# Kernel optimization log

Hardware: AMD Instinct MI355X
Metric: run time of the kernel (lower is better)

The kernel has to match this reference:

```python
import jax, jax.numpy as jnp
import numpy as np

B, S, NCH, OUT = 16384, 256, 8, 2
EPS = 1e-5

def setup_inputs() -> dict:
    key = jax.random.key(0)
    ks = jax.random.split(key, 8)
    scale = 1.0 / np.sqrt(S)
    x = jax.random.normal(ks[0], (B, S, 2 * NCH), dtype=jnp.float32)
    h_0 = jnp.zeros((1,), dtype=jnp.float32)
    # per-channel complex linear weights, stacked: [n_channels, out=S, in=S]
    Wr = jax.random.normal(ks[1], (NCH, S, S), dtype=jnp.float32) * scale
    Wi = jax.random.normal(ks[2], (NCH, S, S), dtype=jnp.float32) * scale
    # final complex linear: [out=OUT//2, in=NCH*S]
    Wfr = jax.random.normal(ks[3], (OUT // 2, NCH * S), dtype=jnp.float32) / np.sqrt(NCH * S)
    Wfi = jax.random.normal(ks[4], (OUT // 2, NCH * S), dtype=jnp.float32) / np.sqrt(NCH * S)
    g_in = jnp.ones((2 * NCH,), dtype=jnp.float32)
    b_in = jnp.zeros((2 * NCH,), dtype=jnp.float32)
    g_out = jnp.ones((OUT,), dtype=jnp.float32)
    b_out = jnp.zeros((OUT,), dtype=jnp.float32)
    return {"x": x, "h_0": h_0, "Wr": Wr, "Wi": Wi, "Wfr": Wfr, "Wfi": Wfi,
            "g_in": g_in, "b_in": b_in, "g_out": g_out, "b_out": b_out}

def reference(x, h_0, Wr, Wi, Wfr, Wfi, g_in, b_in, g_out, b_out):
    # bn_in (training mode): x permuted to [B, 2n, S] in torch -> stats per feature over (B, S)
    mu = jnp.mean(x, axis=(0, 1))
    var = jnp.var(x, axis=(0, 1))  # biased, as torch uses for normalization
    xn = (x - mu) * jax.lax.rsqrt(var + EPS) * g_in + b_in  # [B, S, 2n]
    xi = xn[:, :, 0::2]  # [B, S, n] real parts
    xq = xn[:, :, 1::2]  # [B, S, n] imag parts
    # batched complex linear over channels: y[b,o,c] = sum_s x[b,s,c] W[c,o,s]
    cr = jnp.einsum('bsc,cos->boc', xi, Wr) - jnp.einsum('bsc,cos->boc', xq, Wi)
    ci = jnp.einsum('bsc,cos->boc', xq, Wr) + jnp.einsum('bsc,cos->boc', xi, Wi)
    amp2 = xi * xi + xq * xq  # [B, S, n]
    # channel blocks concatenated along last dim: channel-major ordering
    x_ii = jnp.transpose(amp2 * cr, (0, 2, 1)).reshape(B, NCH * S)
    x_qq = jnp.transpose(amp2 * ci, (0, 2, 1)).reshape(B, NCH * S)
    Cr = x_ii @ Wfr.T - x_qq @ Wfi.T  # [B, OUT//2]
    Ci = x_qq @ Wfr.T + x_ii @ Wfi.T
    y = jnp.concatenate([Cr, Ci], axis=-1)  # [B, OUT]
    mu2 = jnp.mean(y, axis=0)
    var2 = jnp.var(y, axis=0)
    return (y - mu2) * jax.lax.rsqrt(var2 + EPS) * g_out + b_out
```

## Files before the change

kernel.cpp:

```cpp
#include <hip/hip_runtime.h>
#include <stdint.h>

#define B_N   16384
#define S_N   256
#define NCH   8
#define P_N   (B_N * S_N)
#define EPS_F 1e-5f

typedef float  f32x4  __attribute__((ext_vector_type(4)));
typedef __bf16 bf16x8 __attribute__((ext_vector_type(8)));
typedef unsigned int u32x4 __attribute__((ext_vector_type(4)));
typedef unsigned int u32x2 __attribute__((ext_vector_type(2)));

static __device__ __forceinline__ unsigned short f2bf(float f) {
  union { float f; unsigned u; } v; v.f = f;
  unsigned u = v.u;
  u += 0x7fffu + ((u >> 16) & 1u);
  return (unsigned short)(u >> 16);
}
static __device__ __forceinline__ float bf2f(unsigned short h) {
  union { unsigned u; float f; } v; v.u = ((unsigned)h) << 16;
  return v.f;
}

typedef const __attribute__((address_space(1))) unsigned int* gas1_t;
typedef __attribute__((address_space(3))) unsigned int* las3_t;
static __device__ __forceinline__ void gl16(const void* g, void* l) {
  __builtin_amdgcn_global_load_lds((gas1_t)(uintptr_t)g,
                                   (las3_t)(unsigned int)(uintptr_t)l, 16, 0, 0);
}

__global__ __launch_bounds__(256) void pass1_kernel(
    const float* __restrict__ x, unsigned short* __restrict__ xplan,
    float* __restrict__ partials)
{
  __shared__ float ps[4][32];
  const int t = threadIdx.x;
  const int q = t & 3;
  const int pg = t >> 2;
  float s[4] = {0.f,0.f,0.f,0.f}, ss[4] = {0.f,0.f,0.f,0.f};
  const f32x4* xv = (const f32x4*)x;

  for (int it = 0; it < 4; ++it) {
    size_t p0 = ((size_t)blockIdx.x * 4 + it) * 512 + (size_t)pg * 8;
    f32x4 v[8];
    #pragma unroll
    for (int j = 0; j < 8; ++j) v[j] = xv[(p0 + j) * 4 + q];
    #pragma unroll
    for (int j = 0; j < 8; ++j)
      #pragma unroll
      for (int k = 0; k < 4; ++k) { s[k] += v[j][k]; ss[k] += v[j][k] * v[j][k]; }
    #pragma unroll
    for (int j2 = 0; j2 < 4; ++j2) {
      u32x4 w;
      #pragma unroll
      for (int k = 0; k < 4; ++k)
        w[k] = (unsigned)f2bf(v[2*k][j2]) | ((unsigned)f2bf(v[2*k+1][j2]) << 16);
      *(u32x4*)(xplan + (size_t)(q * 4 + j2) * P_N + p0) = w;
    }
  }

  #pragma unroll
  for (int off = 32; off >= 4; off >>= 1) {
    #pragma unroll
    for (int k = 0; k < 4; ++k) { s[k] += __shfl_down(s[k], off); ss[k] += __shfl_down(ss[k], off); }
  }
  const int lane = t & 63, wid = t >> 6;
  if (lane < 4) {
    #pragma unroll
    for (int k = 0; k < 4; ++k) {
      ps[wid][lane * 4 + k]      = s[k];
      ps[wid][16 + lane * 4 + k] = ss[k];
    }
  }
  __syncthreads();
  if (t < 32)
    partials[blockIdx.x * 32 + t] = ps[0][t] + ps[1][t] + ps[2][t] + ps[3][t];
}

__global__ __launch_bounds__(1024) void finalize_kernel(
    const float* __restrict__ partials, const float* __restrict__ g_in,
    const float* __restrict__ b_in, float* __restrict__ AC)
{
  __shared__ float acc[32][32];
  const int t = threadIdx.x;
  const int v = t & 31, chunk = t >> 5;
  float s = 0.f;
  for (int i = 0; i < 64; ++i)
    s += partials[(size_t)(chunk * 64 + i) * 32 + v];
  acc[chunk][v] = s;
  __syncthreads();
  if (t < 32) {
    float tot = 0.f;
    #pragma unroll
    for (int k = 0; k < 32; ++k) tot += acc[k][t];
    acc[0][t] = tot;
  }
  __syncthreads();
  if (t < 16) {
    float n = (float)P_N;
    float mu  = acc[0][t] / n;
    float var = acc[0][16 + t] / n - mu * mu;
    float A = g_in[t] * rsqrtf(var + EPS_F);
    AC[t] = A;
    AC[16 + t] = b_in[t] - mu * A;
  }
}

__global__ __launch_bounds__(256) void wprep_kernel(
    const float* __restrict__ Wr, const float* __restrict__ Wi,
    unsigned short* __restrict__ wr_bf, unsigned short* __restrict__ wi_bf,
    float* __restrict__ RWr, float* __restrict__ RWi)
{
  __shared__ float sr[4], si[4];
  const int row = blockIdx.x, t = threadIdx.x;
  const size_t idx = (size_t)row * 256 + t;
  float vr = Wr[idx], vi = Wi[idx];
  wr_bf[idx] = f2bf(vr);
  wi_bf[idx] = f2bf(vi);
  float rr = vr, ri = vi;
  #pragma unroll
  for (int off = 32; off >= 1; off >>= 1) { rr += __shfl_down(rr, off); ri += __shfl_down(ri, off); }
  if ((t & 63) == 0) { sr[t >> 6] = rr; si[t >> 6] = ri; }
  __syncthreads();
  if (t == 0) {
    RWr[row] = sr[0] + sr[1] + sr[2] + sr[3];
    RWi[row] = si[0] + si[1] + si[2] + si[3];
  }
}

__global__ __launch_bounds__(256) void kterm_kernel(
    const float* __restrict__ AC, const float* __restrict__ RWr, const float* __restrict__ RWi,
    float* __restrict__ Kr, float* __restrict__ Ki)
{
  int idx = blockIdx.x * 256 + threadIdx.x;
  int c = idx >> 8;
  float Ci_ = AC[16 + 2*c], Cq_ = AC[16 + 2*c + 1];
  Kr[idx] = Ci_ * RWr[idx] - Cq_ * RWi[idx];
  Ki[idx] = Cq_ * RWr[idx] + Ci_ * RWi[idx];
}

static __device__ __forceinline__ void issue_w(
    const unsigned short* __restrict__ wr_bf, const unsigned short* __restrict__ wi_bf,
    int c, int u, char* wbuf, int t)
{
  const int oh = u >> 3, c32 = u & 7;
  #pragma unroll
  for (int i = 0; i < 4; ++i) {
    const int L = i * 4096 + t * 16;
    const int row = i * 32 + (t >> 3);
    const int ds_ = (t & 7) ^ (row & 7);
    const unsigned short* wb = (ds_ & 4) ? wi_bf : wr_bf;
    const char* g = (const char*)(wb + (size_t)(c * 256 + oh * 128 + row) * 256
                                     + c32 * 32 + (ds_ & 3) * 8);
    gl16(g, wbuf + L);
  }
}

static __device__ __forceinline__ void issue_x(
    const unsigned short* __restrict__ xplan, int c, int b0, char* xlds, int t)
{
  #pragma unroll
  for (int i = 0; i < 8; ++i) {
    const int plane = i >> 2, si = i & 3;
    const int L = plane * 16384 + si * 4096 + t * 16;
    const int row = si * 8 + (t >> 5);
    const int gd = (t & 31) ^ (row & 7);
    const char* g = (const char*)xplan
        + (((size_t)(2 * c + plane) * P_N + (size_t)(b0 + row) * 256) << 1) + (gd << 4);
    gl16(g, xlds + L);
  }
}

__global__ __launch_bounds__(256, 2) void main_kernel(
    const unsigned short* __restrict__ xplan,
    const unsigned short* __restrict__ wr_bf,
    const unsigned short* __restrict__ wi_bf,
    const float* __restrict__ AC,
    const float* __restrict__ Kr, const float* __restrict__ Ki,
    const float* __restrict__ Wfr, const float* __restrict__ Wfi,
    float* __restrict__ y)
{
  __shared__ char Xlds[32768];
  __shared__ char Wlds[49152];
  float (*red)[32][2] = (float(*)[32][2])Wlds;

  const int t = threadIdx.x;
  const int wid = t >> 6, lane = t & 63;
  const int col = lane & 15, kg = lane >> 4;
  const int b0 = blockIdx.x * 32;

  float pCr[2][4], pCi[2][4];
  #pragma unroll
  for (int m = 0; m < 2; ++m)
    #pragma unroll
    for (int r = 0; r < 4; ++r) { pCr[m][r] = 0.f; pCi[m][r] = 0.f; }

  for (int c = 0; c < NCH; ++c) {
    __builtin_amdgcn_s_barrier();
    issue_x(xplan, c, b0, Xlds, t);
    issue_w(wr_bf, wi_bf, c, 0, Wlds, t);
    int wsel = 0;

    for (int oh = 0; oh < 2; ++oh) {
      f32x4 Srr[2][2], Sqi[2][2], Sqr[2][2], Sii[2][2];
      #pragma unroll
      for (int m = 0; m < 2; ++m)
        #pragma unroll
        for (int n = 0; n < 2; ++n) {
          Srr[m][n] = (f32x4){0.f,0.f,0.f,0.f};
          Sqi[m][n] = (f32x4){0.f,0.f,0.f,0.f};
          Sqr[m][n] = (f32x4){0.f,0.f,0.f,0.f};
          Sii[m][n] = (f32x4){0.f,0.f,0.f,0.f};
        }
      #pragma unroll
      for (int t7 = 0; t7 < 8; ++t7) {
        const int u = oh * 8 + t7;
        const int nsel = (wsel == 2) ? 0 : wsel + 1;
        if (u < 15) {
          issue_w(wr_bf, wi_bf, c, u + 1, Wlds + nsel * 16384, t);
          asm volatile("s_waitcnt vmcnt(4)" ::: "memory");
        } else {
          asm volatile("s_waitcnt vmcnt(0)" ::: "memory");
        }
        __builtin_amdgcn_s_barrier();
        __builtin_amdgcn_sched_barrier(0);

        const int axo = (((t7 * 4 + kg) ^ (col & 7)) << 4);
        bf16x8 ari0 = *(const bf16x8*)(Xlds + col * 512 + axo);
        bf16x8 ari1 = *(const bf16x8*)(Xlds + (16 + col) * 512 + axo);
        bf16x8 aqi0 = *(const bf16x8*)(Xlds + 16384 + col * 512 + axo);
        bf16x8 aqi1 = *(const bf16x8*)(Xlds + 16384 + (16 + col) * 512 + axo);
        const char* Wb = Wlds + wsel * 16384;
        #pragma unroll
        for (int nf = 0; nf < 2; ++nf) {
          const int r = wid * 32 + nf * 16 + col;
          bf16x8 br = *(const bf16x8*)(Wb + r * 128 + (((kg    ) ^ (r & 7)) << 4));
          bf16x8 bi = *(const bf16x8*)(Wb + r * 128 + (((kg + 4) ^ (r & 7)) << 4));
          Srr[0][nf] = __builtin_amdgcn_mfma_f32_16x16x32_bf16(ari0, br, Srr[0][nf], 0,0,0);
          Srr[1][nf] = __builtin_amdgcn_mfma_f32_16x16x32_bf16(ari1, br, Srr[1][nf], 0,0,0);
          Sqr[0][nf] = __builtin_amdgcn_mfma_f32_16x16x32_bf16(aqi0, br, Sqr[0][nf], 0,0,0);
          Sqr[1][nf] = __builtin_amdgcn_mfma_f32_16x16x32_bf16(aqi1, br, Sqr[1][nf], 0,0,0);
          Sii[0][nf] = __builtin_amdgcn_mfma_f32_16x16x32_bf16(ari0, bi, Sii[0][nf], 0,0,0);
          Sii[1][nf] = __builtin_amdgcn_mfma_f32_16x16x32_bf16(ari1, bi, Sii[1][nf], 0,0,0);
          Sqi[0][nf] = __builtin_amdgcn_mfma_f32_16x16x32_bf16(aqi0, bi, Sqi[0][nf], 0,0,0);
          Sqi[1][nf] = __builtin_amdgcn_mfma_f32_16x16x32_bf16(aqi1, bi, Sqi[1][nf], 0,0,0);
        }
        __builtin_amdgcn_sched_barrier(0);
        wsel = nsel;
      }

      const float Ai_ = AC[2*c],      Aq_ = AC[2*c + 1];
      const float Cin = AC[16 + 2*c], Cqn = AC[16 + 2*c + 1];
      #pragma unroll
      for (int nf = 0; nf < 2; ++nf) {
        const int o = oh * 128 + wid * 32 + nf * 16 + col;
        const int gidx = c * 256 + o;
        const float kr = Kr[gidx], ki = Ki[gidx];
        const float wfr = Wfr[gidx], wfi = Wfi[gidx];
        const int og = o >> 3, ob = (o & 7) * 2;
        #pragma unroll
        for (int mf = 0; mf < 2; ++mf) {
          const int bl = mf * 16 + kg * 4;
          #pragma unroll
          for (int r = 0; r < 4; ++r) {
            const int row = bl + r;
            const int sb = row * 512 + ((og ^ (row & 7)) << 4) + ob;
            float xiv = Ai_ * bf2f(*(const unsigned short*)(Xlds + sb)) + Cin;
            float xqv = Aq_ * bf2f(*(const unsigned short*)(Xlds + 16384 + sb)) + Cqn;
            float cr = Ai_ * Srr[mf][nf][r] - Aq_ * Sqi[mf][nf][r] + kr;
            float ci = Aq_ * Sqr[mf][nf][r] + Ai_ * Sii[mf][nf][r] + ki;
            float amp2 = xiv * xiv + xqv * xqv;
            pCr[mf][r] += amp2 * (cr * wfr - ci * wfi);
            pCi[mf][r] += amp2 * (ci * wfr + cr * wfi);
          }
        }
      }
    }
  }

  #pragma unroll
  for (int off = 1; off < 16; off <<= 1) {
    #pragma unroll
    for (int m = 0; m < 2; ++m)
      #pragma unroll
      for (int r = 0; r < 4; ++r) {
        pCr[m][r] += __shfl_xor(pCr[m][r], off);
        pCi[m][r] += __shfl_xor(pCi[m][r], off);
      }
  }
  __syncthreads();
  if (col == 0) {
    #pragma unroll
    for (int m = 0; m < 2; ++m)
      #pragma unroll
      for (int r = 0; r < 4; ++r) {
        red[wid][m*16 + kg*4 + r][0] = pCr[m][r];
        red[wid][m*16 + kg*4 + r][1] = pCi[m][r];
      }
  }
  __syncthreads();
  if (t < 64) {
    int bl = t >> 1, cc = t & 1;
    float v = red[0][bl][cc] + red[1][bl][cc] + red[2][bl][cc] + red[3][bl][cc];
    y[(size_t)(b0 + bl) * 2 + cc] = v;
  }
}

__global__ __launch_bounds__(1024) void ln_kernel(
    const float* __restrict__ y, const float* __restrict__ g_out, const float* __restrict__ b_out,
    float* __restrict__ out)
{
  __shared__ float wsum[16][4];
  __shared__ float st[4];
  const int t = threadIdx.x;
  float s0 = 0.f, q0 = 0.f, s1 = 0.f, q1 = 0.f;
  for (int r = t; r < B_N; r += 1024) {
    float v0 = y[2*r], v1 = y[2*r + 1];
    s0 += v0; q0 += v0 * v0;
    s1 += v1; q1 += v1 * v1;
  }
  #pragma unroll
  for (int off = 32; off >= 1; off >>= 1) {
    s0 += __shfl_down(s0, off); q0 += __shfl_down(q0, off);
    s1 += __shfl_down(s1, off); q1 += __shfl_down(q1, off);
  }
  if ((t & 63) == 0) { int w = t >> 6; wsum[w][0]=s0; wsum[w][1]=q0; wsum[w][2]=s1; wsum[w][3]=q1; }
  __syncthreads();
  if (t == 0) {
    float S0=0.f,Q0=0.f,S1=0.f,Q1=0.f;
    for (int w = 0; w < 16; ++w) { S0+=wsum[w][0]; Q0+=wsum[w][1]; S1+=wsum[w][2]; Q1+=wsum[w][3]; }
    float n = (float)B_N;
    float mu0 = S0 / n, var0 = Q0 / n - mu0 * mu0;
    float mu1 = S1 / n, var1 = Q1 / n - mu1 * mu1;
    st[0] = mu0; st[1] = rsqrtf(var0 + EPS_F);
    st[2] = mu1; st[3] = rsqrtf(var1 + EPS_F);
  }
  __syncthreads();
  float g0 = g_out[0], g1 = g_out[1], bo0 = b_out[0], bo1 = b_out[1];
  float mu0 = st[0], rs0 = st[1], mu1 = st[2], rs1 = st[3];
  for (int r = t; r < B_N; r += 1024) {
    out[2*r]     = (y[2*r]     - mu0) * rs0 * g0 + bo0;
    out[2*r + 1] = (y[2*r + 1] - mu1) * rs1 * g1 + bo1;
  }
}

extern "C" void kernel_launch(void* const* d_in, const int* in_sizes, int n_in,
                              void* d_out, int out_size, void* d_ws, size_t ws_size,
                              hipStream_t stream) {
  (void)in_sizes; (void)n_in; (void)out_size; (void)ws_size;
  const float* x    = (const float*)d_in[0];
  const float* Wr   = (const float*)d_in[2];
  const float* Wi   = (const float*)d_in[3];
  const float* Wfr  = (const float*)d_in[4];
  const float* Wfi  = (const float*)d_in[5];
  const float* g_in = (const float*)d_in[6];
  const float* b_in = (const float*)d_in[7];
  const float* g_out= (const float*)d_in[8];
  const float* b_out= (const float*)d_in[9];
  float* out = (float*)d_out;

  char* ws = (char*)d_ws;
  float* AC    = (float*)(ws + 128);
  float* RWr   = (float*)(ws + 256);
  float* RWi   = (float*)(ws + 256 + 8192);
  float* Kr    = (float*)(ws + 256 + 16384);
  float* Ki    = (float*)(ws + 256 + 24576);
  float* y     = (float*)(ws + 33024);
  float* partials = (float*)(ws + 164096);
  unsigned short* wr_bf = (unsigned short*)(ws + 164096);
  unsigned short* wi_bf = (unsigned short*)(ws + 164096 + 1048576);
  unsigned short* xplan = (unsigned short*)(ws + 2261248);

  pass1_kernel<<<2048, 256, 0, stream>>>(x, xplan, partials);
  finalize_kernel<<<1, 1024, 0, stream>>>(partials, g_in, b_in, AC);
  wprep_kernel<<<2048, 256, 0, stream>>>(Wr, Wi, wr_bf, wi_bf, RWr, RWi);
  kterm_kernel<<<8, 256, 0, stream>>>(AC, RWr, RWi, Kr, Ki);
  main_kernel<<<B_N / 32, 256, 0, stream>>>(xplan, wr_bf, wi_bf, AC, Kr, Ki, Wfr, Wfi, y);
  ln_kernel<<<1, 1024, 0, stream>>>(y, g_out, b_out, out);
}
```

Measured before the change: 201.8 us.

## Retile main kernel to 64-row blocks with unified X/W triple-buffered pipeline

The main kernel now processes 64 batch rows per 512-thread block, and each wave computes a 32x64 output tile. X and W chunks are streamed per 32-wide K phase through a 3-stage LDS ring, using a new interleaved real/imag weight layout written by wprep. Amplitude-squared values are precomputed once into LDS as bf16 rather than recomputed from the full X tile. This halves the weight reloads per batch row and overlaps the X loads with compute, at the cost of more LDS and registers per block, which may lower occupancy.

After: 218.8 us. +8.4%, slower.

```diff
diff --git a/kernel.cpp b/kernel.cpp
--- a/kernel.cpp
+++ b/kernel.cpp
@@ -9,6 +9,7 @@
 
 typedef float  f32x4  __attribute__((ext_vector_type(4)));
 typedef __bf16 bf16x8 __attribute__((ext_vector_type(8)));
+typedef __bf16 bf16x4 __attribute__((ext_vector_type(4)));
 typedef unsigned int u32x4 __attribute__((ext_vector_type(4)));
 typedef unsigned int u32x2 __attribute__((ext_vector_type(2)));
 
@@ -109,15 +110,18 @@
 
 __global__ __launch_bounds__(256) void wprep_kernel(
     const float* __restrict__ Wr, const float* __restrict__ Wi,
-    unsigned short* __restrict__ wr_bf, unsigned short* __restrict__ wi_bf,
+    unsigned short* __restrict__ wp,
     float* __restrict__ RWr, float* __restrict__ RWi)
 {
   __shared__ float sr[4], si[4];
   const int row = blockIdx.x, t = threadIdx.x;
+  const int c = row >> 8, o = row & 255;
   const size_t idx = (size_t)row * 256 + t;
   float vr = Wr[idx], vi = Wi[idx];
-  wr_bf[idx] = f2bf(vr);
-  wi_bf[idx] = f2bf(vi);
+  const int u = t >> 5, g = (t >> 3) & 3, j = t & 7;
+  const size_t base = ((size_t)((c * 8 + u) * 256 + o) << 6) + g * 8 + j;
+  wp[base]      = f2bf(vr);
+  wp[base + 32] = f2bf(vi);
   float rr = vr, ri = vi;
   #pragma unroll
   for (int off = 32; off >= 1; off >>= 1) { rr += __shfl_down(rr, off); ri += __shfl_down(ri, off); }
@@ -140,55 +144,53 @@
   Ki[idx] = Cq_ * RWr[idx] + Ci_ * RWi[idx];
 }
 
-static __device__ __forceinline__ void issue_w(
-    const unsigned short* __restrict__ wr_bf, const unsigned short* __restrict__ wi_bf,
-    int c, int u, char* wbuf, int t)
-{
-  const int oh = u >> 3, c32 = u & 7;
+static __device__ __forceinline__ void issue_phase(
+    const unsigned short* __restrict__ xplan, const unsigned short* __restrict__ wp,
+    int p, int b0, int t, char* xbuf, char* wbuf)
+{
+  const int c = p >> 3, u = p & 7;
+  {
+    const int row = t >> 3, slot = t & 7;
+    const int sd = slot ^ (row & 7);
+    const int pl = sd >> 2, g = sd & 3;
+    const char* gsrc = (const char*)xplan +
+        (((size_t)(2 * c + pl) * P_N + (size_t)(b0 + row) * 256 + u * 32 + g * 8) << 1);
+    gl16(gsrc, xbuf + t * 16);
+  }
   #pragma unroll
   for (int i = 0; i < 4; ++i) {
-    const int L = i * 4096 + t * 16;
-    const int row = i * 32 + (t >> 3);
-    const int ds_ = (t & 7) ^ (row & 7);
-    const unsigned short* wb = (ds_ & 4) ? wi_bf : wr_bf;
-    const char* g = (const char*)(wb + (size_t)(c * 256 + oh * 128 + row) * 256
-                                     + c32 * 32 + (ds_ & 3) * 8);
-    gl16(g, wbuf + L);
-  }
-}
-
-static __device__ __forceinline__ void issue_x(
-    const unsigned short* __restrict__ xplan, int c, int b0, char* xlds, int t)
-{
-  #pragma unroll
-  for (int i = 0; i < 8; ++i) {
-    const int plane = i >> 2, si = i & 3;
-    const int L = plane * 16384 + si * 4096 + t * 16;
-    const int row = si * 8 + (t >> 5);
-    const int gd = (t & 31) ^ (row & 7);
-    const char* g = (const char*)xplan
-        + (((size_t)(2 * c + plane) * P_N + (size_t)(b0 + row) * 256) << 1) + (gd << 4);
-    gl16(g, xlds + L);
-  }
-}
-
-__global__ __launch_bounds__(256, 2) void main_kernel(
+    const int o = i * 64 + (t >> 3), slot = t & 7;
+    const int gd = slot ^ (o & 7);
+    const char* gsrc = (const char*)wp +
+        (((size_t)((c * 8 + u) * 256 + o)) << 7) + (gd << 4);
+    gl16(gsrc, wbuf + i * 8192 + t * 16);
+  }
+}
+
+__global__ __launch_bounds__(512, 2) void main_kernel(
     const unsigned short* __restrict__ xplan,
-    const unsigned short* __restrict__ wr_bf,
-    const unsigned short* __restrict__ wi_bf,
+    const unsigned short* __restrict__ wp,
     const float* __restrict__ AC,
     const float* __restrict__ Kr, const float* __restrict__ Ki,
     const float* __restrict__ Wfr, const float* __restrict__ Wfi,
     float* __restrict__ y)
 {
-  __shared__ char Xlds[32768];
-  __shared__ char Wlds[49152];
-  float (*red)[32][2] = (float(*)[32][2])Wlds;
+  __shared__ char Xc[3][8192];
+  __shared__ char Wc[3][32768];
+  __shared__ unsigned short amp2s[64][256];
+  __shared__ float red[4][64][2];
+  __shared__ float acs[32];
 
   const int t = threadIdx.x;
   const int wid = t >> 6, lane = t & 63;
+  const int mw = wid >> 2, ow = wid & 3;
   const int col = lane & 15, kg = lane >> 4;
-  const int b0 = blockIdx.x * 32;
+  const int c7 = col & 7;
+  const int b0 = blockIdx.x * 64;
+  const int srow = t >> 3, aoq = t & 7;
+  const int ag = aoq >> 1, ah = aoq & 1;
+
+  if (t < 32) acs[t] = AC[t];
 
   float pCr[2][4], pCi[2][4];
   #pragma unroll
@@ -196,83 +198,98 @@
     #pragma unroll
     for (int r = 0; r < 4; ++r) { pCr[m][r] = 0.f; pCi[m][r] = 0.f; }
 
-  for (int c = 0; c < NCH; ++c) {
+  f32x4 acc[2][4][4];
+
+  issue_phase(xplan, wp, 0, b0, t, Xc[0], Wc[0]);
+  issue_phase(xplan, wp, 1, b0, t, Xc[1], Wc[1]);
+
+  float Ai_ = 0.f, Aq_ = 0.f, Cin = 0.f, Cqn = 0.f;
+
+  #pragma unroll 1
+  for (int p = 0; p < 64; ++p) {
+    const int c = p >> 3, u = p & 7;
+    if (p == 63) { asm volatile("s_waitcnt vmcnt(0)" ::: "memory"); }
+    else         { asm volatile("s_waitcnt vmcnt(5)" ::: "memory"); }
     __builtin_amdgcn_s_barrier();
-    issue_x(xplan, c, b0, Xlds, t);
-    issue_w(wr_bf, wi_bf, c, 0, Wlds, t);
-    int wsel = 0;
-
-    for (int oh = 0; oh < 2; ++oh) {
-      f32x4 Srr[2][2], Sqi[2][2], Sqr[2][2], Sii[2][2];
-      #pragma unroll
-      for (int m = 0; m < 2; ++m)
+    if (p + 2 < 64)
+      issue_phase(xplan, wp, p + 2, b0, t, Xc[(p + 2) % 3], Wc[(p + 2) % 3]);
+    __builtin_amdgcn_sched_barrier(0);
+
+    if (u == 0) {
+      Ai_ = acs[2*c]; Aq_ = acs[2*c + 1]; Cin = acs[16 + 2*c]; Cqn = acs[16 + 2*c + 1];
+      #pragma unroll
+      for (int mf = 0; mf < 2; ++mf)
         #pragma unroll
-        for (int n = 0; n < 2; ++n) {
-          Srr[m][n] = (f32x4){0.f,0.f,0.f,0.f};
-          Sqi[m][n] = (f32x4){0.f,0.f,0.f,0.f};
-          Sqr[m][n] = (f32x4){0.f,0.f,0.f,0.f};
-          Sii[m][n] = (f32x4){0.f,0.f,0.f,0.f};
-        }
-      #pragma unroll
-      for (int t7 = 0; t7 < 8; ++t7) {
-        const int u = oh * 8 + t7;
-        const int nsel = (wsel == 2) ? 0 : wsel + 1;
-        if (u < 15) {
-          issue_w(wr_bf, wi_bf, c, u + 1, Wlds + nsel * 16384, t);
-          asm volatile("s_waitcnt vmcnt(4)" ::: "memory");
-        } else {
-          asm volatile("s_waitcnt vmcnt(0)" ::: "memory");
-        }
-        __builtin_amdgcn_s_barrier();
-        __builtin_amdgcn_sched_barrier(0);
-
-        const int axo = (((t7 * 4 + kg) ^ (col & 7)) << 4);
-        bf16x8 ari0 = *(const bf16x8*)(Xlds + col * 512 + axo);
-        bf16x8 ari1 = *(const bf16x8*)(Xlds + (16 + col) * 512 + axo);
-        bf16x8 aqi0 = *(const bf16x8*)(Xlds + 16384 + col * 512 + axo);
-        bf16x8 aqi1 = *(const bf16x8*)(Xlds + 16384 + (16 + col) * 512 + axo);
-        const char* Wb = Wlds + wsel * 16384;
-        #pragma unroll
-        for (int nf = 0; nf < 2; ++nf) {
-          const int r = wid * 32 + nf * 16 + col;
-          bf16x8 br = *(const bf16x8*)(Wb + r * 128 + (((kg    ) ^ (r & 7)) << 4));
-          bf16x8 bi = *(const bf16x8*)(Wb + r * 128 + (((kg + 4) ^ (r & 7)) << 4));
-          Srr[0][nf] = __builtin_amdgcn_mfma_f32_16x16x32_bf16(ari0, br, Srr[0][nf], 0,0,0);
-          Srr[1][nf] = __builtin_amdgcn_mfma_f32_16x16x32_bf16(ari1, br, Srr[1][nf], 0,0,0);
-          Sqr[0][nf] = __builtin_amdgcn_mfma_f32_16x16x32_bf16(aqi0, br, Sqr[0][nf], 0,0,0);
-          Sqr[1][nf] = __builtin_amdgcn_mfma_f32_16x16x32_bf16(aqi1, br, Sqr[1][nf], 0,0,0);
-          Sii[0][nf] = __builtin_amdgcn_mfma_f32_16x16x32_bf16(ari0, bi, Sii[0][nf], 0,0,0);
-          Sii[1][nf] = __builtin_amdgcn_mfma_f32_16x16x32_bf16(ari1, bi, Sii[1][nf], 0,0,0);
-          Sqi[0][nf] = __builtin_amdgcn_mfma_f32_16x16x32_bf16(aqi0, bi, Sqi[0][nf], 0,0,0);
-          Sqi[1][nf] = __builtin_amdgcn_mfma_f32_16x16x32_bf16(aqi1, bi, Sqi[1][nf], 0,0,0);
-        }
-        __builtin_amdgcn_sched_barrier(0);
-        wsel = nsel;
-      }
-
-      const float Ai_ = AC[2*c],      Aq_ = AC[2*c + 1];
-      const float Cin = AC[16 + 2*c], Cqn = AC[16 + 2*c + 1];
-      #pragma unroll
-      for (int nf = 0; nf < 2; ++nf) {
-        const int o = oh * 128 + wid * 32 + nf * 16 + col;
+        for (int nf = 0; nf < 4; ++nf)
+          #pragma unroll
+          for (int s = 0; s < 4; ++s)
+            acc[mf][nf][s] = (f32x4){0.f,0.f,0.f,0.f};
+    }
+
+    const char* Xb = Xc[p % 3];
+    const char* Wb = Wc[p % 3];
+
+    bf16x8 a[2][2];
+    #pragma unroll
+    for (int mf = 0; mf < 2; ++mf)
+      #pragma unroll
+      for (int pl = 0; pl < 2; ++pl) {
+        const int row = mw * 32 + mf * 16 + col;
+        a[mf][pl] = *(const bf16x8*)(Xb + row * 128 + (((pl * 4 + kg) ^ c7) << 4));
+      }
+    bf16x8 b[4][2];
+    #pragma unroll
+    for (int nf = 0; nf < 4; ++nf)
+      #pragma unroll
+      for (int tt = 0; tt < 2; ++tt) {
+        const int o = ow * 64 + nf * 16 + col;
+        b[nf][tt] = *(const bf16x8*)(Wb + o * 128 + (((tt * 4 + kg) ^ c7) << 4));
+      }
+    #pragma unroll
+    for (int mf = 0; mf < 2; ++mf)
+      #pragma unroll
+      for (int nf = 0; nf < 4; ++nf) {
+        acc[mf][nf][0] = __builtin_amdgcn_mfma_f32_16x16x32_bf16(a[mf][0], b[nf][0], acc[mf][nf][0], 0,0,0);
+        acc[mf][nf][1] = __builtin_amdgcn_mfma_f32_16x16x32_bf16(a[mf][1], b[nf][0], acc[mf][nf][1], 0,0,0);
+        acc[mf][nf][2] = __builtin_amdgcn_mfma_f32_16x16x32_bf16(a[mf][0], b[nf][1], acc[mf][nf][2], 0,0,0);
+        acc[mf][nf][3] = __builtin_amdgcn_mfma_f32_16x16x32_bf16(a[mf][1], b[nf][1], acc[mf][nf][3], 0,0,0);
+      }
+
+    {
+      bf16x4 xi = *(const bf16x4*)(Xb + srow * 128 + (((0 + ag) ^ (srow & 7)) << 4) + ah * 8);
+      bf16x4 xq = *(const bf16x4*)(Xb + srow * 128 + (((4 + ag) ^ (srow & 7)) << 4) + ah * 8);
+      unsigned short w[4];
+      #pragma unroll
+      for (int e = 0; e < 4; ++e) {
+        float xiv = Ai_ * (float)xi[e] + Cin;
+        float xqv = Aq_ * (float)xq[e] + Cqn;
+        w[e] = f2bf(xiv * xiv + xqv * xqv);
+      }
+      const int og = u * 32 + aoq * 4;
+      u32x2 pw;
+      pw[0] = (unsigned)w[0] | ((unsigned)w[1] << 16);
+      pw[1] = (unsigned)w[2] | ((unsigned)w[3] << 16);
+      *(u32x2*)((char*)&amp2s[0][0] + srow * 512 + og * 2) = pw;
+    }
+
+    if (u == 7) {
+      __builtin_amdgcn_s_barrier();
+      #pragma unroll
+      for (int nf = 0; nf < 4; ++nf) {
+        const int o = ow * 64 + nf * 16 + col;
         const int gidx = c * 256 + o;
         const float kr = Kr[gidx], ki = Ki[gidx];
         const float wfr = Wfr[gidx], wfi = Wfi[gidx];
-        const int og = o >> 3, ob = (o & 7) * 2;
         #pragma unroll
         for (int mf = 0; mf < 2; ++mf) {
-          const int bl = mf * 16 + kg * 4;
+          const int rb = mw * 32 + mf * 16 + kg * 4;
           #pragma unroll
           for (int r = 0; r < 4; ++r) {
-            const int row = bl + r;
-            const int sb = row * 512 + ((og ^ (row & 7)) << 4) + ob;
-            float xiv = Ai_ * bf2f(*(const unsigned short*)(Xlds + sb)) + Cin;
-            float xqv = Aq_ * bf2f(*(const unsigned short*)(Xlds + 16384 + sb)) + Cqn;
-            float cr = Ai_ * Srr[mf][nf][r] - Aq_ * Sqi[mf][nf][r] + kr;
-            float ci = Aq_ * Sqr[mf][nf][r] + Ai_ * Sii[mf][nf][r] + ki;
-            float amp2 = xiv * xiv + xqv * xqv;
-            pCr[mf][r] += amp2 * (cr * wfr - ci * wfi);
-            pCi[mf][r] += amp2 * (ci * wfr + cr * wfi);
+            float amp = bf2f(amp2s[rb + r][o]);
+            float cr = Ai_ * acc[mf][nf][0][r] - Aq_ * acc[mf][nf][3][r] + kr;
+            float ci = Aq_ * acc[mf][nf][1][r] + Ai_ * acc[mf][nf][2][r] + ki;
+            pCr[mf][r] += amp * (cr * wfr - ci * wfi);
+            pCi[mf][r] += amp * (ci * wfr + cr * wfi);
           }
         }
       }
@@ -289,21 +306,21 @@
         pCi[m][r] += __shfl_xor(pCi[m][r], off);
       }
   }
-  __syncthreads();
   if (col == 0) {
     #pragma unroll
     for (int m = 0; m < 2; ++m)
       #pragma unroll
       for (int r = 0; r < 4; ++r) {
-        red[wid][m*16 + kg*4 + r][0] = pCr[m][r];
-        red[wid][m*16 + kg*4 + r][1] = pCi[m][r];
-      }
-  }
-  __syncthreads();
-  if (t < 64) {
-    int bl = t >> 1, cc = t & 1;
-    float v = red[0][bl][cc] + red[1][bl][cc] + red[2][bl][cc] + red[3][bl][cc];
-    y[(size_t)(b0 + bl) * 2 + cc] = v;
+        const int row = mw * 32 + m * 16 + kg * 4 + r;
+        red[ow][row][0] = pCr[m][r];
+        red[ow][row][1] = pCi[m][r];
+      }
+  }
+  __syncthreads();
+  if (t < 128) {
+    const int row = t >> 1, cc = t & 1;
+    y[(size_t)(b0 + row) * 2 + cc] =
+        red[0][row][cc] + red[1][row][cc] + red[2][row][cc] + red[3][row][cc];
   }
 }
 
@@ -368,14 +385,13 @@
   float* Ki    = (float*)(ws + 256 + 24576);
   float* y     = (float*)(ws + 33024);
   float* partials = (float*)(ws + 164096);
-  unsigned short* wr_bf = (unsigned short*)(ws + 164096);
-  unsigned short* wi_bf = (unsigned short*)(ws + 164096 + 1048576);
+  unsigned short* wp = (unsigned short*)(ws + 164096);
   unsigned short* xplan = (unsigned short*)(ws + 2261248);
 
   pass1_kernel<<<2048, 256, 0, stream>>>(x, xplan, partials);
   finalize_kernel<<<1, 1024, 0, stream>>>(partials, g_in, b_in, AC);
-  wprep_kernel<<<2048, 256, 0, stream>>>(Wr, Wi, wr_bf, wi_bf, RWr, RWi);
+  wprep_kernel<<<2048, 256, 0, stream>>>(Wr, Wi, wp, RWr, RWi);
   kterm_kernel<<<8, 256, 0, stream>>>(AC, RWr, RWi, Kr, Ki);
-  main_kernel<<<B_N / 32, 256, 0, stream>>>(xplan, wr_bf, wi_bf, AC, Kr, Ki, Wfr, Wfi, y);
+  main_kernel<<<B_N / 64, 512, 0, stream>>>(xplan, wp, AC, Kr, Ki, Wfr, Wfi, y);
   ln_kernel<<<1, 1024, 0, stream>>>(y, g_out, b_out, out);
 }
```
